# Performance work log

Measured on AMD Instinct MI355X. Metric: run time of the kernel, lower is better.

The kernel has to match this reference:

```python
import jax, jax.numpy as jnp
import numpy as np

B, T = 8, 512
N_QUBITS, N_ROT, D_PER = 64, 16, 64
D = N_QUBITS * D_PER


def setup_inputs() -> dict:
    key = jax.random.key(0)
    k1, k2, k3, k4 = jax.random.split(key, 4)
    return {
        "x": jax.random.normal(k1, (B, T, D), dtype=jnp.float32),
        "rx_params": jax.random.normal(k2, (N_QUBITS, N_ROT), dtype=jnp.float32),
        "ry_params": jax.random.normal(k3, (N_QUBITS, N_ROT), dtype=jnp.float32),
        "rz_params": jax.random.normal(k4, (N_QUBITS, N_ROT), dtype=jnp.float32),
    }


def _rot_diag(theta, axis):
    # theta: (Q,) per-qubit angle. The torch einsum 'btqd,btqq->btqd' only uses
    # the diagonal of the (Q,Q) rotation matrix. For rx/ry, the paired-qubit
    # construction puts cos(theta_k/2) on both diagonal slots of pair k
    # (first Q//2 angles are used, matching cos[..., :len(idx)]).
    Q = theta.shape[0]
    half = theta[: Q // 2] * 0.5
    if axis in ("x", "y"):
        return jnp.repeat(jnp.cos(half).astype(jnp.complex64), 2)
    # rz: diag(exp(-i a/2), exp(+i a/2)) interleaved over pairs
    e = jnp.exp(-1j * half.astype(jnp.complex64))
    return jnp.stack([e, jnp.conj(e)], axis=-1).reshape(-1)


def _apply_rotation(state, theta, axis):
    # state: (B, T, Q, d_per) complex64
    sf = jnp.fft.fft2(state, axes=(-2, -1))
    sf = sf * _rot_diag(theta, axis)[:, None]  # diagonal per-qubit scale
    return jnp.fft.ifft2(sf, axes=(-2, -1)).real  # torch takes .real


def reference(x, rx_params, ry_params, rz_params):
    b, t, d = x.shape
    q = rx_params.shape[0]
    state = x.reshape(b, t, q, d // q).astype(jnp.complex64)
    for params, axis in ((rx_params, "x"), (ry_params, "y"), (rz_params, "z")):
        theta = params.sum(-1)  # combine n_rotations into one angle per qubit
        state = _apply_rotation(state, theta, axis).astype(jnp.complex64)
    state = state.reshape(b, t, d)
    # noise model: (1 + amp_noise) * exp(i * phase_noise) * state, then L2 norm
    ka, kp = jax.random.split(jax.random.key(42))
    amp = 0.01 * jax.random.normal(ka, state.shape, dtype=jnp.float32)
    ph = 0.005 * jax.random.normal(kp, state.shape, dtype=jnp.float32)
    noisy = (1.0 + amp) * jnp.exp(1j * ph.astype(jnp.complex64)) * state
    norm = jnp.linalg.norm(noisy, axis=-1, keepdims=True)
    noisy = noisy / (norm + 1e-8)
    return jnp.abs(noisy)  # measurement
```

## Files before the change

kernel.cpp:

```cpp
#include <hip/hip_runtime.h>
#include <stdint.h>

typedef _Float16 half8 __attribute__((ext_vector_type(8)));
typedef float floatx4 __attribute__((ext_vector_type(4)));

__device__ __forceinline__ uint32_t rotl32(uint32_t v, int r) {
  return __builtin_amdgcn_alignbit(v, v, 32 - r);
}

__device__ __forceinline__ void threefry2x32(uint32_t k0, uint32_t k1,
                                             uint32_t x0, uint32_t x1,
                                             uint32_t& o0, uint32_t& o1) {
  uint32_t k2 = k0 ^ k1 ^ 0x1BD11BDAu;
  x0 += k0; x1 += k1;
#define TF_R(r) { x0 += x1; x1 = rotl32(x1, (r)); x1 ^= x0; }
  TF_R(13) TF_R(15) TF_R(26) TF_R(6)   x0 += k1; x1 += k2 + 1u;
  TF_R(17) TF_R(29) TF_R(16) TF_R(24)  x0 += k2; x1 += k0 + 2u;
  TF_R(13) TF_R(15) TF_R(26) TF_R(6)   x0 += k0; x1 += k1 + 3u;
  TF_R(17) TF_R(29) TF_R(16) TF_R(24)  x0 += k1; x1 += k2 + 4u;
  TF_R(13) TF_R(15) TF_R(26) TF_R(6)   x0 += k2; x1 += k0 + 5u;
#undef TF_R
  o0 = x0; o1 = x1;
}

__device__ __forceinline__ float noise_mult(uint32_t ka0, uint32_t ka1,
                                            uint32_t idx) {
  uint32_t o0, o1;
  threefry2x32(ka0, ka1, 0u, idx, o0, o1);
  uint32_t bits = o0 ^ o1;
  float vf = __uint_as_float(__builtin_amdgcn_alignbit(0x7Fu, bits, 9));
  float u = fmaxf(fmaf(vf, 2.0f, -3.0f), -0.99999994f);
  float t = fmaf(-u, u, 1.0f);
  float l2 = __log2f(t);
  float p;
  if (__builtin_expect(l2 <= -7.2134752f, 0)) {
    float w = l2 * -0.69314718f;
    float s = sqrtf(w) - 3.0f;
    p = -0.000200214257f;
    p = fmaf(p, s, 0.000100950558f);
    p = fmaf(p, s, 0.00134934322f);
    p = fmaf(p, s, -0.00367342844f);
    p = fmaf(p, s, 0.00573950773f);
    p = fmaf(p, s, -0.0076224613f);
    p = fmaf(p, s, 0.00943887047f);
    p = fmaf(p, s, 1.00167406f);
    p = fmaf(p, s, 2.83297682f);
  } else {
    float a = fmaf(l2, -0.69314718f, -2.5f);
    p = 0.00021858087f;
    p = fmaf(p, a, -0.00125372503f);
    p = fmaf(p, a, -0.00417768164f);
    p = fmaf(p, a, 0.246640727f);
    p = fmaf(p, a, 1.50140941f);
  }
  return fmaf(p, u * 0.014142135623730951f, 1.0f);
}

__device__ __align__(16) _Float16 g_afrag[256 * 16];
__device__ uint32_t g_key[2];

__global__ void setup_kernel(const float* __restrict__ rx,
                             const float* __restrict__ ry,
                             const float* __restrict__ rz) {
  __shared__ float cre[3][64], cim[3][64];
  __shared__ float Gr[64], Gi[64];
  __shared__ float twc[64], tws[64];
  __shared__ float gs[64];
  const int t = threadIdx.x;

  if (t < 32) {
    const float* ps[3] = {rx, ry, rz};
    for (int a = 0; a < 3; ++a) {
      float s = 0.0f;
      for (int r = 0; r < 16; ++r) s += ps[a][t * 16 + r];
      float h = 0.5f * s;
      float ch = cosf(h), sh = sinf(h);
      if (a < 2) {
        cre[a][2 * t] = ch;     cim[a][2 * t] = 0.0f;
        cre[a][2 * t + 1] = ch; cim[a][2 * t + 1] = 0.0f;
      } else {
        cre[2][2 * t] = ch;     cim[2][2 * t] = -sh;
        cre[2][2 * t + 1] = ch; cim[2][2 * t + 1] = sh;
      }
    }
  }
  if (t < 64) {
    double ang = (2.0 * 3.14159265358979323846 / 64.0) * (double)t;
    twc[t] = (float)cos(ang);
    tws[t] = (float)sin(ang);
  }
  __syncthreads();

  if (t < 64) {
    const int k = t, kn = (64 - k) & 63;
    float pr = 1.0f, pi = 0.0f;
    for (int a = 0; a < 3; ++a) {
      float cr = 0.5f * (cre[a][k] + cre[a][kn]);
      float ci = 0.5f * (cim[a][k] - cim[a][kn]);
      float nr = pr * cr - pi * ci;
      float ni = pr * ci + pi * cr;
      pr = nr; pi = ni;
    }
    Gr[k] = pr; Gi[k] = pi;
  }
  __syncthreads();

  if (t < 64) {
    const int mi = t;
    float s = 0.0f;
    for (int k = 0; k < 64; ++k) {
      int idx = (k * mi) & 63;
      s = fmaf(Gr[k], twc[idx], s);
      s = fmaf(-Gi[k], tws[idx], s);
    }
    gs[mi] = s * (1.0f / 64.0f);
  }
  __syncthreads();

  {
    const int w = t >> 6, lane = t & 63, quad = lane >> 4, m = lane & 15;
    const int r0 = 16 * w + m - 8 * quad;
#pragma unroll
    for (int j = 0; j < 8; ++j) {
      g_afrag[t * 16 + j]     = (_Float16)gs[(r0 - j) & 63];
      g_afrag[t * 16 + 8 + j] = (_Float16)gs[(r0 - 32 - j) & 63];
    }
  }

  if (t == 0) {
    uint32_t o0, o1;
    threefry2x32(0u, 42u, 0u, 0u, o0, o1);
    g_key[0] = o0; g_key[1] = o1;
  }
}

__global__ __launch_bounds__(256, 8) void qmain(const float* __restrict__ x,
                                                float* __restrict__ out) {
  __shared__ __align__(16) _Float16 Xt[64 * 72];
  __shared__ float red[4];
  const int tid = threadIdx.x;
  const int row = blockIdx.x;
  const int lane = tid & 63;
  const int w = tid >> 6;
  const int quad = lane >> 4;
  const int m = lane & 15;

  const half8* at = (const half8*)g_afrag;
  half8 af0 = at[2 * tid];
  half8 af1 = at[2 * tid + 1];
  const uint32_t ka0 = g_key[0], ka1 = g_key[1];

  {
    const float* xr = x + (size_t)row * 4096;
    const int d0 = (tid & 31) * 2;
    const int q0 = (tid >> 5) * 8;
    float2 v[8];
#pragma unroll
    for (int s = 0; s < 8; ++s) v[s] = *(const float2*)(xr + (q0 + s) * 64 + d0);
    union { _Float16 h[8]; uint4 u; } r0, r1;
#pragma unroll
    for (int s = 0; s < 8; ++s) { r0.h[s] = (_Float16)v[s].x; r1.h[s] = (_Float16)v[s].y; }
    *(uint4*)&Xt[d0 * 72 + q0] = r0.u;
    *(uint4*)&Xt[(d0 + 1) * 72 + q0] = r1.u;
  }
  __syncthreads();

  floatx4 acc[4];
#pragma unroll
  for (int c = 0; c < 4; ++c) {
    const _Float16* bp = &Xt[(16 * c + m) * 72 + 8 * quad];
    half8 b0 = *(const half8*)bp;
    half8 b1 = *(const half8*)(bp + 32);
    acc[c] = (floatx4){0.0f, 0.0f, 0.0f, 0.0f};
    acc[c] = __builtin_amdgcn_mfma_f32_16x16x32_f16(af0, b0, acc[c], 0, 0, 0);
    acc[c] = __builtin_amdgcn_mfma_f32_16x16x32_f16(af1, b1, acc[c], 0, 0, 0);
  }

  const uint32_t idxbase = ((uint32_t)row << 12) +
                           (uint32_t)(((16 * w + 4 * quad) << 6) + m);
  float ssum = 0.0f;
#pragma unroll
  for (int c = 0; c < 4; ++c) {
#pragma unroll
    for (int r = 0; r < 4; ++r) {
      const uint32_t idx = idxbase + (uint32_t)(r * 64 + 16 * c);
      float val = noise_mult(ka0, ka1, idx) * acc[c][r];
      acc[c][r] = val;
      ssum = fmaf(val, val, ssum);
    }
  }

#pragma unroll
  for (int off = 32; off >= 1; off >>= 1) ssum += __shfl_xor(ssum, off, 64);
  if (lane == 0) red[w] = ssum;
  __syncthreads();
  const float total = red[0] + red[1] + red[2] + red[3];
  const float scale = 1.0f / (sqrtf(total) + 1e-8f);

  float* ob = out + (size_t)row * 4096 + (size_t)(((16 * w + 4 * quad) << 6) + m);
#pragma unroll
  for (int c = 0; c < 4; ++c)
#pragma unroll
    for (int r = 0; r < 4; ++r)
      ob[r * 64 + 16 * c] = fabsf(acc[c][r]) * scale;
}

extern "C" void kernel_launch(void* const* d_in, const int* in_sizes, int n_in,
                              void* d_out, int out_size, void* d_ws, size_t ws_size,
                              hipStream_t stream) {
  const float* x  = (const float*)d_in[0];
  const float* rx = (const float*)d_in[1];
  const float* ry = (const float*)d_in[2];
  const float* rz = (const float*)d_in[3];
  float* out = (float*)d_out;

  setup_kernel<<<1, 256, 0, stream>>>(rx, ry, rz);
  qmain<<<4096, 256, 0, stream>>>(x, out);
}
```

Measured before the change: 137.2 us.

## Split each row across 8 waves instead of 4 with column halves

Raises the block size to 512 threads so each wave computes two of the four 16-column MFMA tiles instead of all four. This halves per-thread work on the threefry-based noise generation and the loads, aiming to expose more parallelism and latency hiding. In exchange it adds more waves per block, a wider reduction across 8 partial sums, and duplicates the A-fragment loads across the two column halves.

```diff
diff --git a/kernel.cpp b/kernel.cpp
--- a/kernel.cpp
+++ b/kernel.cpp
@@ -134,58 +134,62 @@
   }
 }
 
-__global__ __launch_bounds__(256, 8) void qmain(const float* __restrict__ x,
+__global__ __launch_bounds__(512, 6) void qmain(const float* __restrict__ x,
                                                 float* __restrict__ out) {
   __shared__ __align__(16) _Float16 Xt[64 * 72];
-  __shared__ float red[4];
+  __shared__ float red[8];
   const int tid = threadIdx.x;
   const int row = blockIdx.x;
   const int lane = tid & 63;
   const int w = tid >> 6;
+  const int wr = w & 3;
+  const int wc = w >> 2;
   const int quad = lane >> 4;
   const int m = lane & 15;
 
   const half8* at = (const half8*)g_afrag;
-  half8 af0 = at[2 * tid];
-  half8 af1 = at[2 * tid + 1];
+  const int ai = (wr << 6) | lane;
+  half8 af0 = at[2 * ai];
+  half8 af1 = at[2 * ai + 1];
   const uint32_t ka0 = g_key[0], ka1 = g_key[1];
 
   {
     const float* xr = x + (size_t)row * 4096;
     const int d0 = (tid & 31) * 2;
-    const int q0 = (tid >> 5) * 8;
-    float2 v[8];
-#pragma unroll
-    for (int s = 0; s < 8; ++s) v[s] = *(const float2*)(xr + (q0 + s) * 64 + d0);
-    union { _Float16 h[8]; uint4 u; } r0, r1;
-#pragma unroll
-    for (int s = 0; s < 8; ++s) { r0.h[s] = (_Float16)v[s].x; r1.h[s] = (_Float16)v[s].y; }
-    *(uint4*)&Xt[d0 * 72 + q0] = r0.u;
-    *(uint4*)&Xt[(d0 + 1) * 72 + q0] = r1.u;
-  }
-  __syncthreads();
-
-  floatx4 acc[4];
-#pragma unroll
-  for (int c = 0; c < 4; ++c) {
+    const int q0 = (tid >> 5) * 4;
+    float2 v[4];
+#pragma unroll
+    for (int s = 0; s < 4; ++s) v[s] = *(const float2*)(xr + (q0 + s) * 64 + d0);
+    union { _Float16 h[4]; uint2 u; } r0, r1;
+#pragma unroll
+    for (int s = 0; s < 4; ++s) { r0.h[s] = (_Float16)v[s].x; r1.h[s] = (_Float16)v[s].y; }
+    *(uint2*)&Xt[d0 * 72 + q0] = r0.u;
+    *(uint2*)&Xt[(d0 + 1) * 72 + q0] = r1.u;
+  }
+  __syncthreads();
+
+  floatx4 acc[2];
+#pragma unroll
+  for (int cc = 0; cc < 2; ++cc) {
+    const int c = 2 * wc + cc;
     const _Float16* bp = &Xt[(16 * c + m) * 72 + 8 * quad];
     half8 b0 = *(const half8*)bp;
     half8 b1 = *(const half8*)(bp + 32);
-    acc[c] = (floatx4){0.0f, 0.0f, 0.0f, 0.0f};
-    acc[c] = __builtin_amdgcn_mfma_f32_16x16x32_f16(af0, b0, acc[c], 0, 0, 0);
-    acc[c] = __builtin_amdgcn_mfma_f32_16x16x32_f16(af1, b1, acc[c], 0, 0, 0);
+    acc[cc] = (floatx4){0.0f, 0.0f, 0.0f, 0.0f};
+    acc[cc] = __builtin_amdgcn_mfma_f32_16x16x32_f16(af0, b0, acc[cc], 0, 0, 0);
+    acc[cc] = __builtin_amdgcn_mfma_f32_16x16x32_f16(af1, b1, acc[cc], 0, 0, 0);
   }
 
   const uint32_t idxbase = ((uint32_t)row << 12) +
-                           (uint32_t)(((16 * w + 4 * quad) << 6) + m);
+                           (uint32_t)(((16 * wr + 4 * quad) << 6) + (wc << 5) + m);
   float ssum = 0.0f;
 #pragma unroll
-  for (int c = 0; c < 4; ++c) {
+  for (int cc = 0; cc < 2; ++cc) {
 #pragma unroll
     for (int r = 0; r < 4; ++r) {
-      const uint32_t idx = idxbase + (uint32_t)(r * 64 + 16 * c);
-      float val = noise_mult(ka0, ka1, idx) * acc[c][r];
-      acc[c][r] = val;
+      const uint32_t idx = idxbase + (uint32_t)(r * 64 + 16 * cc);
+      float val = noise_mult(ka0, ka1, idx) * acc[cc][r];
+      acc[cc][r] = val;
       ssum = fmaf(val, val, ssum);
     }
   }
@@ -194,15 +198,18 @@
   for (int off = 32; off >= 1; off >>= 1) ssum += __shfl_xor(ssum, off, 64);
   if (lane == 0) red[w] = ssum;
   __syncthreads();
-  const float total = red[0] + red[1] + red[2] + red[3];
+  float total = 0.0f;
+#pragma unroll
+  for (int i = 0; i < 8; ++i) total += red[i];
   const float scale = 1.0f / (sqrtf(total) + 1e-8f);
 
-  float* ob = out + (size_t)row * 4096 + (size_t)(((16 * w + 4 * quad) << 6) + m);
-#pragma unroll
-  for (int c = 0; c < 4; ++c)
+  float* ob = out + (size_t)row * 4096 +
+              (size_t)(((16 * wr + 4 * quad) << 6) + (wc << 5) + m);
+#pragma unroll
+  for (int cc = 0; cc < 2; ++cc)
 #pragma unroll
     for (int r = 0; r < 4; ++r)
-      ob[r * 64 + 16 * c] = fabsf(acc[c][r]) * scale;
+      ob[r * 64 + 16 * cc] = fabsf(acc[cc][r]) * scale;
 }
 
 extern "C" void kernel_launch(void* const* d_in, const int* in_sizes, int n_in,
@@ -215,5 +222,5 @@
   float* out = (float*)d_out;
 
   setup_kernel<<<1, 256, 0, stream>>>(rx, ry, rz);
-  qmain<<<4096, 256, 0, stream>>>(x, out);
-}
+  qmain<<<4096, 512, 0, stream>>>(x, out);
+}
```

Result: no change. 137.4 us (+0.1%).
